# Optimization experiments

Measured on AMD Instinct MI355X. Metric: run time of the kernel, lower is better.

The kernel has to match this reference:

```python
import jax, jax.numpy as jnp
import numpy as np

B, N_PER, P_PER = 64, 64, 2016   # graphs, nodes/graph, pairs/graph (C(64,2))
IN_DIM, HID, OUT = 64, 128, 10
EDGE_P = 0.125


def _build_graph_structures():
    """Integer preprocessing replicating build_2sets_from_embeddings's
    combinatorics (pairs, iso_type source, triangle-based 2-set edges)."""
    rng = np.random.default_rng(0)
    n, b = N_PER, B
    A = rng.random((b, n, n)) < EDGE_P
    A = np.triu(A, 1)
    A = A | A.transpose(0, 2, 1)                      # symmetric, no self loops
    gs, us, vs = np.nonzero(A)                        # directed edges, both dirs
    edge_index = np.stack([gs * n + us, gs * n + vs]).astype(np.int64)
    batch = np.repeat(np.arange(b), n).astype(np.int64)
    iu, iv = np.triu_indices(n, 1)                    # local pair (u<v) lists
    pidx = np.full((n, n), -1, np.int64)
    pidx[iu, iv] = np.arange(P_PER)
    pidx[iv, iu] = np.arange(P_PER)                   # symmetric lookup = sorted()
    pair_u = (np.arange(b)[:, None] * n + iu[None, :]).ravel().astype(np.int64)
    pair_v = (np.arange(b)[:, None] * n + iv[None, :]).ravel().astype(np.int64)
    iso_type = A[:, iu, iv].astype(np.float32).ravel()[:, None]  # [B*P_PER,1]
    # 2-set edges: pair (u,v) -> sorted(v,w) and sorted(u,w) for every common
    # neighbor w of u and v (matches _build_2set_edges exactly)
    common = A[:, iu, :] & A[:, iv, :]                # (B, P_PER, n)
    g2, ps, ws = np.nonzero(common)
    u, v = iu[ps], iv[ps]
    d1 = pidx[v, ws]
    d2 = pidx[u, ws]
    src = np.concatenate([g2 * P_PER + ps, g2 * P_PER + ps])
    dst = np.concatenate([g2 * P_PER + d1, g2 * P_PER + d2])
    two_edges = np.stack([src, dst]).astype(np.int64)
    two_batch = np.repeat(np.arange(b), P_PER).astype(np.int64)
    return edge_index, batch, pair_u, pair_v, iso_type, two_edges, two_batch


def setup_inputs() -> dict:
    ei, batch, pu, pv, iso, te, tb = _build_graph_structures()
    key = jax.random.key(0)
    ks = jax.random.split(key, 16)
    w = lambda k, i, o: jax.random.normal(k, (i, o), jnp.float32) / np.float32(np.sqrt(i))
    two_in = 2 * HID + 1
    return {
        "x": jax.random.normal(ks[0], (B * N_PER, IN_DIM), jnp.float32),
        "g1_W1_0": w(ks[1], IN_DIM, HID), "g1_W2_0": w(ks[2], IN_DIM, HID),
        "g1_W1_1": w(ks[3], HID, HID),    "g1_W2_1": w(ks[4], HID, HID),
        "g1_W1_2": w(ks[5], HID, HID),    "g1_W2_2": w(ks[6], HID, HID),
        "k_W1_0": w(ks[7], two_in, HID),  "k_W2_0": w(ks[8], two_in, HID),
        "k_W1_1": w(ks[9], HID, HID),     "k_W2_1": w(ks[10], HID, HID),
        "c_W0": w(ks[11], 2 * HID, HID),  "c_b0": jnp.zeros((HID,), jnp.float32),
        "c_W1": w(ks[12], HID, OUT),      "c_b1": jnp.zeros((OUT,), jnp.float32),
        "iso_type": jnp.asarray(iso),
        "edge_index": jnp.asarray(ei), "batch": jnp.asarray(batch),
        "pair_u": jnp.asarray(pu), "pair_v": jnp.asarray(pv),
        "two_edges": jnp.asarray(te), "two_batch": jnp.asarray(tb),
    }


def _mp_layer(h, ei, W1, W2):
    # relu( h @ W1 + scatter_add_{dst}( h[src] @ W2 ) )  -- OneGNNLayer / KSetLayer
    msg = h[ei[0]] @ W2
    agg = jax.ops.segment_sum(msg, ei[1], num_segments=h.shape[0])
    return jax.nn.relu(h @ W1 + agg)


def reference(x, g1_W1_0, g1_W2_0, g1_W1_1, g1_W2_1, g1_W1_2, g1_W2_2,
              k_W1_0, k_W2_0, k_W1_1, k_W2_1,
              c_W0, c_b0, c_W1, c_b1,
              iso_type, edge_index, batch, pair_u, pair_v, two_edges, two_batch):
    h = _mp_layer(x, edge_index, g1_W1_0, g1_W2_0)
    h = _mp_layer(h, edge_index, g1_W1_1, g1_W2_1)
    h = _mp_layer(h, edge_index, g1_W1_2, g1_W2_2)
    graph_emb_1 = jax.ops.segment_sum(h, batch, num_segments=B)
    # 2-set features: [h_u, h_v, iso_type]  -> [P, 2H+1]
    two_x = jnp.concatenate([h[pair_u], h[pair_v], iso_type], axis=1)
    h2 = _mp_layer(two_x, two_edges, k_W1_0, k_W2_0)
    h2 = _mp_layer(h2, two_edges, k_W1_1, k_W2_1)
    graph_emb_2 = jax.ops.segment_sum(h2, two_batch, num_segments=B)
    combined = jnp.concatenate([graph_emb_1, graph_emb_2], axis=1)
    hc = jax.nn.relu(combined @ c_W0 + c_b0)   # Dropout(p=0.5) inactive in eval
    return hc @ c_W1 + c_b1
```

## Files before the change

kernel.cpp:

```cpp
#include <hip/hip_runtime.h>
#include <hip/hip_bf16.h>


typedef short s16x8 __attribute__((ext_vector_type(8)));
typedef float f32x4 __attribute__((ext_vector_type(4)));

__device__ __forceinline__ unsigned short f2bf(float f) {
  union { float f; unsigned u; } x; x.f = f;
  unsigned r = (x.u + 0x7fffu + ((x.u >> 16) & 1u)) >> 16;
  return (unsigned short)r;
}
__device__ __forceinline__ float bf2f(unsigned short h) {
  union { unsigned u; float f; } x; x.u = ((unsigned)h) << 16;
  return x.f;
}
__device__ __forceinline__ float4 ldbf4(const unsigned short* p) {
  ushort4 q = *(const ushort4*)p;
  return make_float4(bf2f(q.x), bf2f(q.y), bf2f(q.z), bf2f(q.w));
}
__device__ __forceinline__ void stbf4(unsigned short* p, float4 v) {
  ushort4 q;
  q.x = f2bf(v.x); q.y = f2bf(v.y); q.z = f2bf(v.z); q.w = f2bf(v.w);
  *(ushort4*)p = q;
}
__device__ __forceinline__ float4 ld4(const float* p) { return *(const float4*)p; }

template<int KCS, int ASTR>
__device__ __forceinline__ void mfma_dual_lds(
    const unsigned short* A, const unsigned short* Wfrag,
    f32x4 (&accA)[8], f32x4 (&accB)[8])
{
  const int lane = threadIdx.x & 63;
  const int wv = threadIdx.x >> 6;
  const int row = wv * 16 + (lane & 15);
  const int k0 = (lane >> 4) << 3;
  const unsigned short* ap = A + row * ASTR + k0;
  const unsigned short* wp = Wfrag + (size_t)lane * 8;
#pragma unroll
  for (int i = 0; i < 8; ++i) { accA[i] = (f32x4)0.f; accB[i] = (f32x4)0.f; }
#pragma unroll
  for (int kc = 0; kc < KCS; ++kc) {
    s16x8 af = *(const s16x8*)(ap + kc * 32);
#pragma unroll
    for (int nt = 0; nt < 8; ++nt) {
      s16x8 b0 = *(const s16x8*)(wp + ((size_t)((nt)*KCS + kc) << 9));
      s16x8 b1 = *(const s16x8*)(wp + ((size_t)((8 + nt) * KCS + kc) << 9));
      accA[nt] = __builtin_amdgcn_mfma_f32_16x16x32_bf16(af, b0, accA[nt], 0, 0, 0);
      accB[nt] = __builtin_amdgcn_mfma_f32_16x16x32_bf16(af, b1, accB[nt], 0, 0, 0);
    }
  }
}

template<int KCS, int ASTR>
__device__ __forceinline__ void mfma_dual_lds16(
    const unsigned short* A, const unsigned short* Wfrag,
    f32x4 (&accA)[2], f32x4 (&accB)[2])
{
  const int lane = threadIdx.x & 63;
  const int w16 = threadIdx.x >> 6;
  const int rw = w16 & 3, ch = w16 >> 2;
  const int row = rw * 16 + (lane & 15);
  const int k0 = (lane >> 4) << 3;
  const unsigned short* ap = A + row * ASTR + k0;
  const unsigned short* wp = Wfrag + (size_t)lane * 8;
  accA[0] = (f32x4)0.f; accA[1] = (f32x4)0.f;
  accB[0] = (f32x4)0.f; accB[1] = (f32x4)0.f;
  __builtin_amdgcn_s_setprio(1);
#pragma unroll
  for (int kc = 0; kc < KCS; ++kc) {
    s16x8 af = *(const s16x8*)(ap + kc * 32);
#pragma unroll
    for (int n2 = 0; n2 < 2; ++n2) {
      int nt = ch * 2 + n2;
      s16x8 b0 = *(const s16x8*)(wp + ((size_t)(nt * KCS + kc) << 9));
      s16x8 b1 = *(const s16x8*)(wp + ((size_t)((8 + nt) * KCS + kc) << 9));
      accA[n2] = __builtin_amdgcn_mfma_f32_16x16x32_bf16(af, b0, accA[n2], 0, 0, 0);
      accB[n2] = __builtin_amdgcn_mfma_f32_16x16x32_bf16(af, b1, accB[n2], 0, 0, 0);
    }
  }
  __builtin_amdgcn_s_setprio(0);
}

__device__ __forceinline__ void epi_lds16(const f32x4 (&accA)[2], const f32x4 (&accB)[2],
    unsigned short (*preS)[136], unsigned short (*msgS)[136])
{
  const int lane = threadIdx.x & 63;
  const int w16 = threadIdx.x >> 6;
  const int rw = w16 & 3, ch = w16 >> 2;
  const int col = lane & 15;
  const int r0 = rw * 16 + ((lane >> 4) << 2);
  __syncthreads();
#pragma unroll
  for (int n2 = 0; n2 < 2; ++n2) {
    int nt = ch * 2 + n2;
#pragma unroll
    for (int r = 0; r < 4; ++r) {
      preS[r0 + r][nt * 16 + col] = f2bf(accA[n2][r]);
      msgS[r0 + r][nt * 16 + col] = f2bf(accB[n2][r]);
    }
  }
  __syncthreads();
}

__device__ __forceinline__ void epi_global(const f32x4 (&accA)[8], const f32x4 (&accB)[8],
    unsigned short (*sOut)[136], unsigned short* Ca, unsigned short* Cb, long tile)
{
  const int tid = threadIdx.x;
  const int lane = tid & 63;
  const int wv = tid >> 6;
  const int col = lane & 15;
  const int r0 = wv * 16 + ((lane >> 4) << 2);
  const long rowBase = tile * 64;
#pragma unroll
  for (int sel = 0; sel < 2; ++sel) {
    __syncthreads();
#pragma unroll
    for (int nt = 0; nt < 8; ++nt) {
#pragma unroll
      for (int r = 0; r < 4; ++r)
        sOut[r0 + r][nt * 16 + col] = f2bf(sel ? accB[nt][r] : accA[nt][r]);
    }
    __syncthreads();
    unsigned short* C = sel ? Cb : Ca;
#pragma unroll
    for (int i = 0; i < 4; ++i) {
      int fi = tid + i * 256;
      int row = fi >> 4;
      int c8 = fi & 15;
      *(uint4*)(C + (rowBase + row) * 128 + c8 * 8) = *(uint4*)&sOut[row][c8 * 8];
    }
  }
}

struct NArgs {
  const float* x;
  const int* ei;
  const int* gstart;
  const unsigned short *Wf0, *Wf1, *Wf2;
  unsigned short* Hn;
  float* ge1;
  int E1;
};

__global__ __launch_bounds__(1024) void node_stage(NArgs a)
{
  __shared__ __align__(16) unsigned short hS[64][136];
  __shared__ __align__(16) unsigned short preS[64][136];
  __shared__ __align__(16) unsigned short msgS[64][136];
  __shared__ int ldeg[64], lcur[64], loff[65];
  __shared__ unsigned short ledge[1024];
  __shared__ float sge[128];

  const int b = blockIdx.x;
  const int t = threadIdx.x;
  const int base = b * 64;

  const int es = a.gstart[b], ee = a.gstart[b + 1];
  if (t < 64) ldeg[t] = 0;
  if (t < 128) sge[t] = 0.f;
  __syncthreads();
  for (int i = es + t; i < ee; i += 1024)
    atomicAdd(&ldeg[a.ei[a.E1 + i] - base], 1);
  __syncthreads();
  if (t < 64) {
    int v = ldeg[t], s = v;
#pragma unroll
    for (int d = 1; d < 64; d <<= 1) {
      int o = __shfl_up(s, d, 64);
      if (t >= d) s += o;
    }
    loff[t] = s - v;
    lcur[t] = s - v;
    if (t == 63) loff[64] = s;
  }
  unsigned short* xs = &preS[0][0];
  for (int i = t; i < 64 * 64; i += 1024) {
    int r = i >> 6, c = i & 63;
    xs[r * 72 + c] = f2bf(a.x[(size_t)(base + r) * 64 + c]);
  }
  __syncthreads();
  for (int i = es + t; i < ee; i += 1024) {
    int s = a.ei[i] - base, d = a.ei[a.E1 + i] - base;
    int pos = atomicAdd(&lcur[d], 1);
    ledge[pos] = (unsigned short)s;
  }
  __syncthreads();

  f32x4 accA[2], accB[2];
  const int grp = t >> 5, f = (t & 31) * 4;

  mfma_dual_lds16<2, 72>(xs, a.Wf0, accA, accB);
  epi_lds16(accA, accB, preS, msgS);
  for (int r = grp; r < 64; r += 32) {
    float4 acc = ldbf4(&preS[r][f]);
    int j1 = loff[r + 1];
    for (int j = loff[r]; j < j1; ++j) {
      float4 m = ldbf4(&msgS[ledge[j]][f]);
      acc.x += m.x; acc.y += m.y; acc.z += m.z; acc.w += m.w;
    }
    stbf4(&hS[r][f], make_float4(fmaxf(acc.x, 0.f), fmaxf(acc.y, 0.f),
                                 fmaxf(acc.z, 0.f), fmaxf(acc.w, 0.f)));
  }
  __syncthreads();

  mfma_dual_lds16<4, 136>(&hS[0][0], a.Wf1, accA, accB);
  epi_lds16(accA, accB, preS, msgS);
  for (int r = grp; r < 64; r += 32) {
    float4 acc = ldbf4(&preS[r][f]);
    int j1 = loff[r + 1];
    for (int j = loff[r]; j < j1; ++j) {
      float4 m = ldbf4(&msgS[ledge[j]][f]);
      acc.x += m.x; acc.y += m.y; acc.z += m.z; acc.w += m.w;
    }
    stbf4(&hS[r][f], make_float4(fmaxf(acc.x, 0.f), fmaxf(acc.y, 0.f),
                                 fmaxf(acc.z, 0.f), fmaxf(acc.w, 0.f)));
  }
  __syncthreads();

  mfma_dual_lds16<4, 136>(&hS[0][0], a.Wf2, accA, accB);
  epi_lds16(accA, accB, preS, msgS);
  {
    float4 g = make_float4(0.f, 0.f, 0.f, 0.f);
    for (int r = grp; r < 64; r += 32) {
      float4 acc = ldbf4(&preS[r][f]);
      int j1 = loff[r + 1];
      for (int j = loff[r]; j < j1; ++j) {
        float4 m = ldbf4(&msgS[ledge[j]][f]);
        acc.x += m.x; acc.y += m.y; acc.z += m.z; acc.w += m.w;
      }
      float4 o = make_float4(fmaxf(acc.x, 0.f), fmaxf(acc.y, 0.f),
                             fmaxf(acc.z, 0.f), fmaxf(acc.w, 0.f));
      stbf4(&hS[r][f], o);
      g.x += o.x; g.y += o.y; g.z += o.z; g.w += o.w;
    }
    atomicAdd(&sge[f + 0], g.x);
    atomicAdd(&sge[f + 1], g.y);
    atomicAdd(&sge[f + 2], g.z);
    atomicAdd(&sge[f + 3], g.w);
  }
  __syncthreads();
  if (t < 128) a.ge1[b * 128 + t] = sge[t];
  {
    int row = t >> 4, c8 = t & 15;
    *(uint4*)(a.Hn + (size_t)(base + row) * 128 + c8 * 8) = *(uint4*)&hS[row][c8 * 8];
  }
}

__global__ __launch_bounds__(256) void hv_gemm(
    const unsigned short* __restrict__ Hn,
    const unsigned short* __restrict__ Wf3, const unsigned short* __restrict__ Wf4,
    unsigned short* __restrict__ HU1, unsigned short* __restrict__ HU2,
    unsigned short* __restrict__ HV1, unsigned short* __restrict__ HV2)
{
  __shared__ __align__(16) unsigned short hS[64][136];
  const int g = blockIdx.x >> 1;
  const int sel = blockIdx.x & 1;
  const int tid = threadIdx.x;
  const unsigned short* src = Hn + (size_t)g * 64 * 128;
#pragma unroll
  for (int i = 0; i < 4; ++i) {
    int fi = tid + i * 256;
    int row = fi >> 4, c8 = fi & 15;
    *(uint4*)&hS[row][c8 * 8] = *(const uint4*)(src + row * 128 + c8 * 8);
  }
  __syncthreads();
  f32x4 accA[8], accB[8];
  mfma_dual_lds<4, 136>(&hS[0][0], sel ? Wf4 : Wf3, accA, accB);
  epi_global(accA, accB, hS, sel ? HV1 : HU1, sel ? HV2 : HU2, g);
}

struct PrepArgs {
  const float* wa[6];
  const float* wb[6];
  unsigned short* Wf[6];
  const int* te; int E2;
  int* degP;
  const int* ei; int E1;
  int* gstart;
  int nCnt;
};

__global__ void prep(PrepArgs p)
{
  int bb = blockIdx.x, t = threadIdx.x;
  if (bb < 88) {
    int gid = bb * 256 + t;
    if (gid < 22528) {
      int pi, local, kcs, kclog;
      if (gid < 2048) { pi = 0; local = gid; kcs = 2; kclog = 1; }
      else { int r = gid - 2048; pi = 1 + (r >> 12); local = r & 4095; kcs = 4; kclog = 2; }
      int lane = local & 63;
      int t1 = local >> 6;
      int kc = t1 & (kcs - 1);
      int t2 = t1 >> kclog;
      int nt = t2 & 7;
      int wsel = t2 >> 3;
      const float* W = wsel ? p.wb[pi] : p.wa[pi];
      int k0 = kc * 32 + ((lane >> 4) << 3);
      int n = nt * 16 + (lane & 15);
      unsigned short tmp[8];
#pragma unroll
      for (int j = 0; j < 8; ++j) tmp[j] = f2bf(W[(size_t)(k0 + j) * 128 + n]);
      *(uint4*)(p.Wf[pi] + (size_t)local * 8) = *(uint4*)tmp;
    }
  } else if (bb < 88 + p.nCnt) {
    int e = (bb - 88) * 256 + t;
    if (e < p.E2) atomicAdd(&p.degP[p.te[p.E2 + e]], 1);
  } else {
    int e = (bb - 88 - p.nCnt) * 256 + t;
    if (e <= p.E1) {
      int ge = (e < p.E1) ? (p.ei[e] >> 6) : 64;
      int gp = (e > 0) ? (p.ei[e - 1] >> 6) : -1;
      for (int g = gp + 1; g <= ge; ++g) p.gstart[g] = e;
    }
  }
}

__global__ __launch_bounds__(256) void scan_reduce(const int* __restrict__ deg,
                                                   int* __restrict__ bsum, int n)
{
  __shared__ int s[256];
  int b = blockIdx.x, t = threadIdx.x;
  int base = b * 1024;
  int v = 0;
#pragma unroll
  for (int i = 0; i < 4; ++i) {
    int idx = base + t + i * 256;
    if (idx < n) v += deg[idx];
  }
  s[t] = v;
  __syncthreads();
  for (int d = 128; d > 0; d >>= 1) {
    if (t < d) s[t] += s[t + d];
    __syncthreads();
  }
  if (t == 0) bsum[b] = s[0];
}

__global__ __launch_bounds__(1024) void scan_partials(int* __restrict__ bsum, int nb)
{
  __shared__ int s[1024];
  int t = threadIdx.x;
  s[t] = (t < nb) ? bsum[t] : 0;
  __syncthreads();
  for (int d = 1; d < 1024; d <<= 1) {
    int v = (t >= d) ? s[t - d] : 0;
    __syncthreads();
    s[t] += v;
    __syncthreads();
  }
  if (t < nb) bsum[t] = (t == 0) ? 0 : s[t - 1];
  if (t == 1023) bsum[nb] = s[1023];
}

__global__ __launch_bounds__(256) void scan_final(const int* __restrict__ deg,
                                                  const int* __restrict__ bsum,
                                                  int* __restrict__ off,
                                                  int* __restrict__ cur, int n, int nb)
{
  __shared__ int s[256];
  int b = blockIdx.x, t = threadIdx.x;
  int base = b * 1024 + t * 4;
  int v0 = 0, v1 = 0, v2 = 0, v3 = 0;
  if (base + 0 < n) v0 = deg[base + 0];
  if (base + 1 < n) v1 = deg[base + 1];
  if (base + 2 < n) v2 = deg[base + 2];
  if (base + 3 < n) v3 = deg[base + 3];
  s[t] = v0 + v1 + v2 + v3;
  __syncthreads();
  for (int d = 1; d < 256; d <<= 1) {
    int v = (t >= d) ? s[t - d] : 0;
    __syncthreads();
    s[t] += v;
    __syncthreads();
  }
  int run = bsum[b] + ((t == 0) ? 0 : s[t - 1]);
  if (base + 0 < n) { off[base + 0] = run; cur[base + 0] = run; run += v0; }
  if (base + 1 < n) { off[base + 1] = run; cur[base + 1] = run; run += v1; }
  if (base + 2 < n) { off[base + 2] = run; cur[base + 2] = run; run += v2; }
  if (base + 3 < n) { off[base + 3] = run; cur[base + 3] = run; run += v3; }
  if (b == 0 && t == 0) off[n] = bsum[nb];
}

__global__ void csr_fill_pair(const int* __restrict__ te, int E2,
                              const int* __restrict__ pu, const int* __restrict__ pv,
                              const float* __restrict__ iso,
                              int* __restrict__ curP, int4* __restrict__ recP)
{
  int e = blockIdx.x * 256 + threadIdx.x;
  if (e >= E2) return;
  int s = te[e], d = te[E2 + e];
  int pos = atomicAdd(&curP[d], 1);
  recP[pos] = make_int4(pu[s], pv[s], __float_as_int(iso[s]), s);
}

__global__ __launch_bounds__(256) void gather_two0_bf(
    const unsigned short* __restrict__ HU1, const unsigned short* __restrict__ HV1,
    const unsigned short* __restrict__ HU2, const unsigned short* __restrict__ HV2,
    const float* __restrict__ iso,
    const float* __restrict__ w1iso, const float* __restrict__ w2iso,
    const int* __restrict__ pu, const int* __restrict__ pv,
    const int* __restrict__ off, const int4* __restrict__ rec,
    unsigned short* __restrict__ out, int P)
{
  int blk = (int)blockIdx.x;
  const int nB = (int)gridDim.x;
  if ((nB & 7) == 0)
    blk = (blk & 7) * (nB >> 3) + (blk >> 3);
  int p = blk * 8 + (threadIdx.x >> 5);
  if (p >= P) return;
  int f = (threadIdx.x & 31) * 4;
  float4 wi1 = ld4(w1iso + f);
  float4 wi2 = ld4(w2iso + f);
  int u0 = pu[p], v0 = pv[p];
  float is0 = iso[p];
  float4 a = ldbf4(HU1 + (size_t)u0 * 128 + f);
  float4 b = ldbf4(HV1 + (size_t)v0 * 128 + f);
  float4 acc;
  acc.x = a.x + b.x + is0 * wi1.x;
  acc.y = a.y + b.y + is0 * wi1.y;
  acc.z = a.z + b.z + is0 * wi1.z;
  acc.w = a.w + b.w + is0 * wi1.w;
  int j = off[p], e1 = off[p + 1];
  for (; j + 1 < e1; j += 2) {
    int4 r0 = rec[j], r1 = rec[j + 1];
    float4 mu0 = ldbf4(HU2 + (size_t)r0.x * 128 + f);
    float4 mv0 = ldbf4(HV2 + (size_t)r0.y * 128 + f);
    float4 mu1 = ldbf4(HU2 + (size_t)r1.x * 128 + f);
    float4 mv1 = ldbf4(HV2 + (size_t)r1.y * 128 + f);
    float i0 = __int_as_float(r0.z), i1 = __int_as_float(r1.z);
    acc.x += mu0.x + mv0.x + i0 * wi2.x + mu1.x + mv1.x + i1 * wi2.x;
    acc.y += mu0.y + mv0.y + i0 * wi2.y + mu1.y + mv1.y + i1 * wi2.y;
    acc.z += mu0.z + mv0.z + i0 * wi2.z + mu1.z + mv1.z + i1 * wi2.z;
    acc.w += mu0.w + mv0.w + i0 * wi2.w + mu1.w + mv1.w + i1 * wi2.w;
  }
  if (j < e1) {
    int4 r0 = rec[j];
    float4 mu0 = ldbf4(HU2 + (size_t)r0.x * 128 + f);
    float4 mv0 = ldbf4(HV2 + (size_t)r0.y * 128 + f);
    float i0 = __int_as_float(r0.z);
    acc.x += mu0.x + mv0.x + i0 * wi2.x;
    acc.y += mu0.y + mv0.y + i0 * wi2.y;
    acc.z += mu0.z + mv0.z + i0 * wi2.z;
    acc.w += mu0.w + mv0.w + i0 * wi2.w;
  }
  stbf4(out + (size_t)p * 128 + f,
        make_float4(fmaxf(acc.x, 0.f), fmaxf(acc.y, 0.f),
                    fmaxf(acc.z, 0.f), fmaxf(acc.w, 0.f)));
}

__global__ __launch_bounds__(64) void pair_l1(
    const unsigned short* __restrict__ H2,
    const unsigned short* __restrict__ Wfrag,
    const int* __restrict__ off, const int4* __restrict__ rec,
    float* __restrict__ gep)
{
  __shared__ __align__(16) unsigned short hS[16][136];
  __shared__ int offS[17];
  __shared__ int recwS[256];
  __shared__ float sge[128];

  const int tid = threadIdx.x;
  int qt = (int)blockIdx.x;
  const int nB = (int)gridDim.x;
  if ((nB & 7) == 0)
    qt = (qt & 7) * (nB >> 3) + (qt >> 3);
  const int r0 = qt * 16;

  if (tid < 17) offS[tid] = off[r0 + tid];
  sge[tid] = 0.f;
  sge[tid + 64] = 0.f;

  {
    const unsigned short* src = H2 + (size_t)r0 * 128;
#pragma unroll
    for (int i = 0; i < 4; ++i) {
      int fi = tid + i * 64;
      int row = fi >> 4, c8 = fi & 15;
      *(uint4*)&hS[row][c8 * 8] = *(const uint4*)(src + row * 128 + c8 * 8);
    }
  }
  __syncthreads();

  const int e0 = offS[0];
  const int ecnt = offS[16] - e0;
  const bool useS = (ecnt <= 256);
  if (useS)
    for (int j = tid; j < ecnt; j += 64) recwS[j] = rec[e0 + j].w;

  const int lane = tid;
  const int arow = lane & 15;
  const int k0 = (lane >> 4) << 3;
  const unsigned short* hp = &hS[0][0] + arow * 136 + k0;
  const unsigned short* wp = Wfrag + (size_t)lane * 8;
  f32x4 acc[8];
#pragma unroll
  for (int nt = 0; nt < 8; ++nt) acc[nt] = (f32x4)0.f;
  __builtin_amdgcn_s_setprio(1);
#pragma unroll
  for (int kc = 0; kc < 4; ++kc) {
    s16x8 ah = *(const s16x8*)(hp + kc * 32);
#pragma unroll
    for (int nt = 0; nt < 8; ++nt) {
      s16x8 b0 = *(const s16x8*)(wp + ((size_t)(nt * 4 + kc) << 9));
      acc[nt] = __builtin_amdgcn_mfma_f32_16x16x32_bf16(ah, b0, acc[nt], 0, 0, 0);
    }
  }
  __builtin_amdgcn_s_setprio(0);
  __syncthreads();

  {
    const int grp = tid >> 5, f = (tid & 31) * 4;
    for (int i = grp; i < 16; i += 2) {
      float4 a = make_float4(0.f, 0.f, 0.f, 0.f);
      int j = offS[i], e1 = offS[i + 1];
      for (; j + 1 < e1; j += 2) {
        int s0 = useS ? recwS[j - e0] : rec[j].w;
        int s1 = useS ? recwS[j + 1 - e0] : rec[j + 1].w;
        float4 m0 = ldbf4(H2 + (size_t)s0 * 128 + f);
        float4 m1 = ldbf4(H2 + (size_t)s1 * 128 + f);
        a.x += m0.x + m1.x; a.y += m0.y + m1.y;
        a.z += m0.z + m1.z; a.w += m0.w + m1.w;
      }
      if (j < e1) {
        int s0 = useS ? recwS[j - e0] : rec[j].w;
        float4 m0 = ldbf4(H2 + (size_t)s0 * 128 + f);
        a.x += m0.x; a.y += m0.y; a.z += m0.z; a.w += m0.w;
      }
      stbf4(&hS[i][f], a);
    }
  }
  __syncthreads();

  __builtin_amdgcn_s_setprio(1);
#pragma unroll
  for (int kc = 0; kc < 4; ++kc) {
    s16x8 ag = *(const s16x8*)(hp + kc * 32);
#pragma unroll
    for (int nt = 0; nt < 8; ++nt) {
      s16x8 b1 = *(const s16x8*)(wp + ((size_t)((8 + nt) * 4 + kc) << 9));
      acc[nt] = __builtin_amdgcn_mfma_f32_16x16x32_bf16(ag, b1, acc[nt], 0, 0, 0);
    }
  }
  __builtin_amdgcn_s_setprio(0);

  const int col0 = lane & 15;
#pragma unroll
  for (int nt = 0; nt < 8; ++nt) {
    float s = fmaxf(acc[nt][0], 0.f) + fmaxf(acc[nt][1], 0.f)
            + fmaxf(acc[nt][2], 0.f) + fmaxf(acc[nt][3], 0.f);
    atomicAdd(&sge[nt * 16 + col0], s);
  }
  __syncthreads();
  gep[(size_t)qt * 128 + tid] = sge[tid];
  gep[(size_t)qt * 128 + tid + 64] = sge[tid + 64];
}

__global__ void classifier(const float* __restrict__ ge1, const float* __restrict__ gep,
                           const float* __restrict__ W0, const float* __restrict__ b0,
                           const float* __restrict__ W1, const float* __restrict__ b1,
                           float* __restrict__ out)
{
  __shared__ float comb[256];
  __shared__ float hc[128];
  int g = blockIdx.x, t = threadIdx.x;
  comb[t] = ge1[g * 128 + t];
  float s2 = 0.f;
  const float* gpr = gep + (size_t)g * 126 * 128 + t;
  for (int i = 0; i < 126; ++i) s2 += gpr[i * 128];
  comb[t + 128] = s2;
  __syncthreads();
  float s = b0[t];
  for (int k = 0; k < 256; ++k) s += comb[k] * W0[k * 128 + t];
  hc[t] = fmaxf(s, 0.f);
  __syncthreads();
  if (t < 10) {
    float s2o = b1[t];
    for (int k = 0; k < 128; ++k) s2o += hc[k] * W1[k * 10 + t];
    out[g * 10 + t] = s2o;
  }
}

extern "C" void kernel_launch(void* const* d_in, const int* in_sizes, int n_in,
                              void* d_out, int out_size, void* d_ws, size_t ws_size,
                              hipStream_t stream)
{
  (void)n_in; (void)out_size; (void)ws_size;
  const float* x       = (const float*)d_in[0];
  const float* g1_W1_0 = (const float*)d_in[1];
  const float* g1_W2_0 = (const float*)d_in[2];
  const float* g1_W1_1 = (const float*)d_in[3];
  const float* g1_W2_1 = (const float*)d_in[4];
  const float* g1_W1_2 = (const float*)d_in[5];
  const float* g1_W2_2 = (const float*)d_in[6];
  const float* k_W1_0  = (const float*)d_in[7];
  const float* k_W2_0  = (const float*)d_in[8];
  const float* k_W1_1  = (const float*)d_in[9];
  const float* k_W2_1  = (const float*)d_in[10];
  const float* c_W0    = (const float*)d_in[11];
  const float* c_b0    = (const float*)d_in[12];
  const float* c_W1    = (const float*)d_in[13];
  const float* c_b1    = (const float*)d_in[14];
  const float* iso     = (const float*)d_in[15];
  const int*   ei      = (const int*)d_in[16];
  const int*   pu      = (const int*)d_in[18];
  const int*   pv      = (const int*)d_in[19];
  const int*   te      = (const int*)d_in[20];

  const int N  = in_sizes[0] / 64;
  const int E1 = in_sizes[16] / 2;
  const int P  = in_sizes[18];
  const int E2 = in_sizes[20] / 2;
  const int B  = 64;
  const int nTiles = P / 64;

  const size_t NH = (size_t)N * 128;
  const size_t PH = (size_t)P * 128;

  float* ge1 = (float*)d_ws;
  float* gep = ge1 + 8192;
  unsigned short* HU1 = (unsigned short*)(gep + (size_t)4 * nTiles * 128);
  unsigned short* HV1 = HU1 + NH;
  unsigned short* HU2 = HV1 + NH;
  unsigned short* HV2 = HU2 + NH;
  unsigned short* H2   = HV2 + NH;
  unsigned short* Hn   = H2 + PH;
  unsigned short* Wf0  = Hn + NH;
  unsigned short* Wf1  = Wf0 + 16384;
  unsigned short* Wf2  = Wf1 + 32768;
  unsigned short* Wf3  = Wf2 + 32768;
  unsigned short* Wf4  = Wf3 + 32768;
  unsigned short* Wf5  = Wf4 + 32768;

  size_t ipOff = ((size_t)((char*)(Wf5 + 32768) - (char*)d_ws) + 15) & ~(size_t)15;
  int4* recP   = (int4*)((char*)d_ws + ipOff);
  int* degP    = (int*)(recP + E2);
  int* offP    = degP + P;
  int* curP    = offP + P + 1;
  int* bsumP   = curP + P;
  int* gstartN = bsumP + 128;

  const int nbP  = (P + 1023) / 1024;
  const int nCnt = (E2 + 255) / 256;
  const int nBnd = (E1 + 256) / 256;

  hipMemsetAsync(degP, 0, (size_t)P * 4, stream);

  PrepArgs pa;
  pa.wa[0] = g1_W1_0;           pa.wb[0] = g1_W2_0;
  pa.wa[1] = g1_W1_1;           pa.wb[1] = g1_W2_1;
  pa.wa[2] = g1_W1_2;           pa.wb[2] = g1_W2_2;
  pa.wa[3] = k_W1_0;            pa.wb[3] = k_W2_0;
  pa.wa[4] = k_W1_0 + 128*128;  pa.wb[4] = k_W2_0 + 128*128;
  pa.wa[5] = k_W1_1;            pa.wb[5] = k_W2_1;
  pa.Wf[0] = Wf0; pa.Wf[1] = Wf1; pa.Wf[2] = Wf2;
  pa.Wf[3] = Wf3; pa.Wf[4] = Wf4; pa.Wf[5] = Wf5;
  pa.te = te; pa.E2 = E2; pa.degP = degP;
  pa.ei = ei; pa.E1 = E1; pa.gstart = gstartN; pa.nCnt = nCnt;
  prep<<<88 + nCnt + nBnd, 256, 0, stream>>>(pa);

  scan_reduce<<<nbP, 256, 0, stream>>>(degP, bsumP, P);
  scan_partials<<<1, 1024, 0, stream>>>(bsumP, nbP);
  scan_final<<<nbP, 256, 0, stream>>>(degP, bsumP, offP, curP, P, nbP);
  csr_fill_pair<<<nCnt, 256, 0, stream>>>(te, E2, pu, pv, iso, curP, recP);

  NArgs na;
  na.x = x; na.ei = ei; na.gstart = gstartN; na.E1 = E1;
  na.Wf0 = Wf0; na.Wf1 = Wf1; na.Wf2 = Wf2;
  na.Hn = Hn; na.ge1 = ge1;
  node_stage<<<B, 1024, 0, stream>>>(na);

  hv_gemm<<<2 * B, 256, 0, stream>>>(Hn, Wf3, Wf4, HU1, HU2, HV1, HV2);

  gather_two0_bf<<<(P + 7) / 8, 256, 0, stream>>>(HU1, HV1, HU2, HV2, iso,
                                                  k_W1_0 + 256 * 128, k_W2_0 + 256 * 128,
                                                  pu, pv, offP, recP, H2, P);

  pair_l1<<<nTiles * 4, 64, 0, stream>>>(H2, Wf5, offP, recP, gep);

  classifier<<<B, 128, 0, stream>>>(ge1, gep, c_W0, c_b0, c_W1, c_b1, (float*)d_out);
}
```

Before: 278.8 us.

## Fuse preprocessing, scan and CSR fill into one cooperative kernel with grid syncs

Replaces the memset, the prep kernel, the three-kernel prefix scan and the CSR fill with a single cooperative kernel of 512 blocks. Grid-wide syncs separate the stages, and the cross-block scan partials are summed serially by each block's first thread. This removes several kernel launches and their gaps, at the cost of grid-sync overhead and less parallelism inside each stage.

```diff
diff --git a/kernel.cpp b/kernel.cpp
--- a/kernel.cpp
+++ b/kernel.cpp
@@ -1,5 +1,8 @@
 #include <hip/hip_runtime.h>
 #include <hip/hip_bf16.h>
+#include <hip/hip_cooperative_groups.h>
+
+namespace cg = cooperative_groups;
 
 
 typedef short s16x8 __attribute__((ext_vector_type(8)));
@@ -269,7 +272,7 @@
   epi_global(accA, accB, hS, sel ? HV1 : HU1, sel ? HV2 : HU2, g);
 }
 
-struct PrepArgs {
+struct CoopArgs {
   const float* wa[6];
   const float* wb[6];
   unsigned short* Wf[6];
@@ -277,121 +280,105 @@
   int* degP;
   const int* ei; int E1;
   int* gstart;
-  int nCnt;
+  const int* pu; const int* pv; const float* iso;
+  int* offP; int* curP; int* bsumP;
+  int4* recP;
+  int P;
 };
 
-__global__ void prep(PrepArgs p)
-{
-  int bb = blockIdx.x, t = threadIdx.x;
-  if (bb < 88) {
-    int gid = bb * 256 + t;
-    if (gid < 22528) {
-      int pi, local, kcs, kclog;
-      if (gid < 2048) { pi = 0; local = gid; kcs = 2; kclog = 1; }
-      else { int r = gid - 2048; pi = 1 + (r >> 12); local = r & 4095; kcs = 4; kclog = 2; }
-      int lane = local & 63;
-      int t1 = local >> 6;
-      int kc = t1 & (kcs - 1);
-      int t2 = t1 >> kclog;
-      int nt = t2 & 7;
-      int wsel = t2 >> 3;
-      const float* W = wsel ? p.wb[pi] : p.wa[pi];
-      int k0 = kc * 32 + ((lane >> 4) << 3);
-      int n = nt * 16 + (lane & 15);
-      unsigned short tmp[8];
-#pragma unroll
-      for (int j = 0; j < 8; ++j) tmp[j] = f2bf(W[(size_t)(k0 + j) * 128 + n]);
-      *(uint4*)(p.Wf[pi] + (size_t)local * 8) = *(uint4*)tmp;
-    }
-  } else if (bb < 88 + p.nCnt) {
-    int e = (bb - 88) * 256 + t;
-    if (e < p.E2) atomicAdd(&p.degP[p.te[p.E2 + e]], 1);
-  } else {
-    int e = (bb - 88 - p.nCnt) * 256 + t;
-    if (e <= p.E1) {
-      int ge = (e < p.E1) ? (p.ei[e] >> 6) : 64;
-      int gp = (e > 0) ? (p.ei[e - 1] >> 6) : -1;
-      for (int g = gp + 1; g <= ge; ++g) p.gstart[g] = e;
-    }
-  }
-}
-
-__global__ __launch_bounds__(256) void scan_reduce(const int* __restrict__ deg,
-                                                   int* __restrict__ bsum, int n)
-{
+__global__ __launch_bounds__(256) void coop_prep(CoopArgs p)
+{
+  cg::grid_group grid = cg::this_grid();
   __shared__ int s[256];
-  int b = blockIdx.x, t = threadIdx.x;
-  int base = b * 1024;
-  int v = 0;
-#pragma unroll
-  for (int i = 0; i < 4; ++i) {
-    int idx = base + t + i * 256;
-    if (idx < n) v += deg[idx];
-  }
-  s[t] = v;
-  __syncthreads();
-  for (int d = 128; d > 0; d >>= 1) {
-    if (t < d) s[t] += s[t + d];
+  __shared__ int basePfx;
+  const int t = threadIdx.x;
+  const int gtid = blockIdx.x * 256 + t;
+  const int gsz = gridDim.x * 256;
+  const int nb = (p.P + 1023) / 1024;
+
+  for (int i = gtid; i < p.P; i += gsz) p.degP[i] = 0;
+  for (int gid = gtid; gid < 22528; gid += gsz) {
+    int pi, local, kcs, kclog;
+    if (gid < 2048) { pi = 0; local = gid; kcs = 2; kclog = 1; }
+    else { int r = gid - 2048; pi = 1 + (r >> 12); local = r & 4095; kcs = 4; kclog = 2; }
+    int lane = local & 63;
+    int t1 = local >> 6;
+    int kc = t1 & (kcs - 1);
+    int t2 = t1 >> kclog;
+    int nt = t2 & 7;
+    int wsel = t2 >> 3;
+    const float* W = wsel ? p.wb[pi] : p.wa[pi];
+    int k0 = kc * 32 + ((lane >> 4) << 3);
+    int n = nt * 16 + (lane & 15);
+    unsigned short tmp[8];
+#pragma unroll
+    for (int j = 0; j < 8; ++j) tmp[j] = f2bf(W[(size_t)(k0 + j) * 128 + n]);
+    *(uint4*)(p.Wf[pi] + (size_t)local * 8) = *(uint4*)tmp;
+  }
+  for (int e = gtid; e <= p.E1; e += gsz) {
+    int ge = (e < p.E1) ? (p.ei[e] >> 6) : 64;
+    int gp = (e > 0) ? (p.ei[e - 1] >> 6) : -1;
+    for (int g = gp + 1; g <= ge; ++g) p.gstart[g] = e;
+  }
+  grid.sync();
+
+  for (int e = gtid; e < p.E2; e += gsz) atomicAdd(&p.degP[p.te[p.E2 + e]], 1);
+  grid.sync();
+
+  if ((int)blockIdx.x < nb) {
+    int base = blockIdx.x * 1024;
+    int v = 0;
+#pragma unroll
+    for (int i = 0; i < 4; ++i) {
+      int idx = base + t + i * 256;
+      if (idx < p.P) v += p.degP[idx];
+    }
+    s[t] = v;
     __syncthreads();
-  }
-  if (t == 0) bsum[b] = s[0];
-}
-
-__global__ __launch_bounds__(1024) void scan_partials(int* __restrict__ bsum, int nb)
-{
-  __shared__ int s[1024];
-  int t = threadIdx.x;
-  s[t] = (t < nb) ? bsum[t] : 0;
-  __syncthreads();
-  for (int d = 1; d < 1024; d <<= 1) {
-    int v = (t >= d) ? s[t - d] : 0;
+    for (int d = 128; d > 0; d >>= 1) {
+      if (t < d) s[t] += s[t + d];
+      __syncthreads();
+    }
+    if (t == 0) p.bsumP[blockIdx.x] = s[0];
+  }
+  grid.sync();
+
+  if ((int)blockIdx.x < nb) {
+    int b = blockIdx.x;
+    if (t == 0) {
+      int acc = 0;
+      for (int k = 0; k < b; ++k) acc += p.bsumP[k];
+      basePfx = acc;
+    }
     __syncthreads();
-    s[t] += v;
+    int base = b * 1024 + t * 4;
+    int v0 = 0, v1 = 0, v2 = 0, v3 = 0;
+    if (base + 0 < p.P) v0 = p.degP[base + 0];
+    if (base + 1 < p.P) v1 = p.degP[base + 1];
+    if (base + 2 < p.P) v2 = p.degP[base + 2];
+    if (base + 3 < p.P) v3 = p.degP[base + 3];
+    s[t] = v0 + v1 + v2 + v3;
     __syncthreads();
-  }
-  if (t < nb) bsum[t] = (t == 0) ? 0 : s[t - 1];
-  if (t == 1023) bsum[nb] = s[1023];
-}
-
-__global__ __launch_bounds__(256) void scan_final(const int* __restrict__ deg,
-                                                  const int* __restrict__ bsum,
-                                                  int* __restrict__ off,
-                                                  int* __restrict__ cur, int n, int nb)
-{
-  __shared__ int s[256];
-  int b = blockIdx.x, t = threadIdx.x;
-  int base = b * 1024 + t * 4;
-  int v0 = 0, v1 = 0, v2 = 0, v3 = 0;
-  if (base + 0 < n) v0 = deg[base + 0];
-  if (base + 1 < n) v1 = deg[base + 1];
-  if (base + 2 < n) v2 = deg[base + 2];
-  if (base + 3 < n) v3 = deg[base + 3];
-  s[t] = v0 + v1 + v2 + v3;
-  __syncthreads();
-  for (int d = 1; d < 256; d <<= 1) {
-    int v = (t >= d) ? s[t - d] : 0;
-    __syncthreads();
-    s[t] += v;
-    __syncthreads();
-  }
-  int run = bsum[b] + ((t == 0) ? 0 : s[t - 1]);
-  if (base + 0 < n) { off[base + 0] = run; cur[base + 0] = run; run += v0; }
-  if (base + 1 < n) { off[base + 1] = run; cur[base + 1] = run; run += v1; }
-  if (base + 2 < n) { off[base + 2] = run; cur[base + 2] = run; run += v2; }
-  if (base + 3 < n) { off[base + 3] = run; cur[base + 3] = run; run += v3; }
-  if (b == 0 && t == 0) off[n] = bsum[nb];
-}
-
-__global__ void csr_fill_pair(const int* __restrict__ te, int E2,
-                              const int* __restrict__ pu, const int* __restrict__ pv,
-                              const float* __restrict__ iso,
-                              int* __restrict__ curP, int4* __restrict__ recP)
-{
-  int e = blockIdx.x * 256 + threadIdx.x;
-  if (e >= E2) return;
-  int s = te[e], d = te[E2 + e];
-  int pos = atomicAdd(&curP[d], 1);
-  recP[pos] = make_int4(pu[s], pv[s], __float_as_int(iso[s]), s);
+    for (int d = 1; d < 256; d <<= 1) {
+      int v = (t >= d) ? s[t - d] : 0;
+      __syncthreads();
+      s[t] += v;
+      __syncthreads();
+    }
+    int run = basePfx + ((t == 0) ? 0 : s[t - 1]);
+    if (base + 0 < p.P) { p.offP[base + 0] = run; p.curP[base + 0] = run; run += v0; }
+    if (base + 1 < p.P) { p.offP[base + 1] = run; p.curP[base + 1] = run; run += v1; }
+    if (base + 2 < p.P) { p.offP[base + 2] = run; p.curP[base + 2] = run; run += v2; }
+    if (base + 3 < p.P) { p.offP[base + 3] = run; p.curP[base + 3] = run; run += v3; }
+    if (b == nb - 1 && t == 0) p.offP[p.P] = basePfx + p.bsumP[b];
+  }
+  grid.sync();
+
+  for (int e = gtid; e < p.E2; e += gsz) {
+    int sp = p.te[e], d = p.te[p.E2 + e];
+    int pos = atomicAdd(&p.curP[d], 1);
+    p.recP[pos] = make_int4(p.pu[sp], p.pv[sp], __float_as_int(p.iso[sp]), sp);
+  }
 }
 
 __global__ __launch_bounds__(256) void gather_two0_bf(
@@ -640,29 +627,23 @@
   int* bsumP   = curP + P;
   int* gstartN = bsumP + 128;
 
-  const int nbP  = (P + 1023) / 1024;
-  const int nCnt = (E2 + 255) / 256;
-  const int nBnd = (E1 + 256) / 256;
-
-  hipMemsetAsync(degP, 0, (size_t)P * 4, stream);
-
-  PrepArgs pa;
-  pa.wa[0] = g1_W1_0;           pa.wb[0] = g1_W2_0;
-  pa.wa[1] = g1_W1_1;           pa.wb[1] = g1_W2_1;
-  pa.wa[2] = g1_W1_2;           pa.wb[2] = g1_W2_2;
-  pa.wa[3] = k_W1_0;            pa.wb[3] = k_W2_0;
-  pa.wa[4] = k_W1_0 + 128*128;  pa.wb[4] = k_W2_0 + 128*128;
-  pa.wa[5] = k_W1_1;            pa.wb[5] = k_W2_1;
-  pa.Wf[0] = Wf0; pa.Wf[1] = Wf1; pa.Wf[2] = Wf2;
-  pa.Wf[3] = Wf3; pa.Wf[4] = Wf4; pa.Wf[5] = Wf5;
-  pa.te = te; pa.E2 = E2; pa.degP = degP;
-  pa.ei = ei; pa.E1 = E1; pa.gstart = gstartN; pa.nCnt = nCnt;
-  prep<<<88 + nCnt + nBnd, 256, 0, stream>>>(pa);
-
-  scan_reduce<<<nbP, 256, 0, stream>>>(degP, bsumP, P);
-  scan_partials<<<1, 1024, 0, stream>>>(bsumP, nbP);
-  scan_final<<<nbP, 256, 0, stream>>>(degP, bsumP, offP, curP, P, nbP);
-  csr_fill_pair<<<nCnt, 256, 0, stream>>>(te, E2, pu, pv, iso, curP, recP);
+  CoopArgs ca;
+  ca.wa[0] = g1_W1_0;           ca.wb[0] = g1_W2_0;
+  ca.wa[1] = g1_W1_1;           ca.wb[1] = g1_W2_1;
+  ca.wa[2] = g1_W1_2;           ca.wb[2] = g1_W2_2;
+  ca.wa[3] = k_W1_0;            ca.wb[3] = k_W2_0;
+  ca.wa[4] = k_W1_0 + 128*128;  ca.wb[4] = k_W2_0 + 128*128;
+  ca.wa[5] = k_W1_1;            ca.wb[5] = k_W2_1;
+  ca.Wf[0] = Wf0; ca.Wf[1] = Wf1; ca.Wf[2] = Wf2;
+  ca.Wf[3] = Wf3; ca.Wf[4] = Wf4; ca.Wf[5] = Wf5;
+  ca.te = te; ca.E2 = E2; ca.degP = degP;
+  ca.ei = ei; ca.E1 = E1; ca.gstart = gstartN;
+  ca.pu = pu; ca.pv = pv; ca.iso = iso;
+  ca.offP = offP; ca.curP = curP; ca.bsumP = bsumP;
+  ca.recP = recP; ca.P = P;
+  void* kargs[] = { &ca };
+  hipLaunchCooperativeKernel((const void*)coop_prep, dim3(512), dim3(256),
+                             kargs, 0, stream);
 
   NArgs na;
   na.x = x; na.ei = ei; na.gstart = gstartN; na.E1 = E1;
```

Result: slower. 551.0 us (+97.6%).
